# Optimization experiments

Hardware: AMD Instinct MI355X
Metric: run time of the kernel (lower is better)

## Reference

```python
import jax, jax.numpy as jnp
import numpy as np

MU = 1.0  # opts.loss_type[1]


def setup_inputs() -> dict:
    key = jax.random.key(0)
    k1, k2 = jax.random.split(key)
    B, D, N = 8, 3, 4096
    srcs = jax.random.normal(k1, (B, D, N), dtype=jnp.float32)
    tgts = jax.random.normal(k2, (B, D, N), dtype=jnp.float32)
    return {"srcs": srcs, "tgts": tgts}


def reference(srcs, tgts):
    # [B, D, N] -> [B, N, D]
    s = jnp.transpose(srcs, (0, 2, 1))
    t = jnp.transpose(tgts, (0, 2, 1))
    # squared euclidean pairwise distances: ||s_i - t_j||^2, [B, N, M]
    s_sq = jnp.sum(s * s, axis=-1)          # [B, N]
    t_sq = jnp.sum(t * t, axis=-1)          # [B, M]
    cross = jnp.einsum('bnd,bmd->bnm', s, t)  # [B, N, M]
    P = s_sq[:, :, None] + t_sq[:, None, :] - 2.0 * cross
    # bidirectional chamfer mins
    d_tgt = jnp.min(P, axis=1)  # min over src points, [B, M]
    d_src = jnp.min(P, axis=2)  # min over tgt points, [B, N]
    distances = jnp.stack([d_tgt, d_src], axis=-1)  # [B, N, 2]
    # Geman-McClure robust penalty
    losses = (MU * distances / (distances + MU)).sum(axis=2).mean(axis=1).mean()
    return losses
```

## Files before the change

### kernel.cpp

```cpp
#include <hip/hip_runtime.h>


#define NPTS 4096
#define NB   8

typedef __attribute__((ext_vector_type(8)))  short bf16x8;
typedef __attribute__((ext_vector_type(16))) float floatx16;

#define OFF_APACK_S 0u
#define OFF_APACK_T (1u << 20)
#define OFF_BPACK_S (2u << 20)
#define OFF_BPACK_T (3u << 20)
#define OFF_BSUM    (4u << 20)

union V16 { int4 i; bf16x8 h; };

__device__ __forceinline__ unsigned short f2bf(float f) {
    unsigned u = __float_as_uint(f);
    u += 0x7FFFu + ((u >> 16) & 1u);
    return (unsigned short)(u >> 16);
}
__device__ __forceinline__ float bf2f(unsigned short h) {
    return __uint_as_float(((unsigned)h) << 16);
}
__device__ __forceinline__ int pk(unsigned short lo, unsigned short hi) {
    return (int)((unsigned)lo | ((unsigned)hi << 16));
}

__device__ __forceinline__ void pack_point(const float* __restrict__ cloud,
                                           int b, int j, int gid,
                                           char* __restrict__ apack,
                                           char* __restrict__ bpack) {
    const unsigned short ONE = 0x3F80;
    const float* p = cloud + b * 3 * NPTS;
    const float x = p[j], y = p[NPTS + j], z = p[2 * NPTS + j];
    const unsigned short hx = f2bf(x), hy = f2bf(y), hz = f2bf(z);
    const unsigned short lx = f2bf(x - bf2f(hx));
    const unsigned short ly = f2bf(y - bf2f(hy));
    const unsigned short lz = f2bf(z - bf2f(hz));
    const unsigned short a0 = f2bf(-2.0f * bf2f(hx));
    const unsigned short a1 = f2bf(-2.0f * bf2f(hy));
    const unsigned short a2 = f2bf(-2.0f * bf2f(hz));
    const unsigned short m0 = f2bf(-2.0f * (x - bf2f(hx)));
    const unsigned short m1 = f2bf(-2.0f * (y - bf2f(hy)));
    const unsigned short m2 = f2bf(-2.0f * (z - bf2f(hz)));
    const float n2 = fmaf(z, z, fmaf(y, y, x * x));
    const unsigned short n2h = f2bf(n2);
    const unsigned short n2l = f2bf(n2 - bf2f(n2h));

    int4* Ap = (int4*)(apack + (size_t)gid * 32);
    Ap[0] = make_int4(pk(a0, a1), pk(a2, m0), pk(m1, m2), pk(a0, a1));
    Ap[1] = make_int4(pk(a2, n2h), pk(n2l, ONE), pk(ONE, 0), 0);

    int4* Bp = (int4*)(bpack + (size_t)gid * 32);
    Bp[0] = make_int4(pk(hx, hy), pk(hz, hx), pk(hy, hz), pk(lx, ly));
    Bp[1] = make_int4(pk(lz, ONE), pk(ONE, n2h), pk(n2l, 0), 0);
}

__global__ __launch_bounds__(256)
void transform_kernel(const float* __restrict__ srcs,
                      const float* __restrict__ tgts,
                      char* __restrict__ ws) {
    const int gid = blockIdx.x * 256 + threadIdx.x;
    const int b = gid >> 12, j = gid & 4095;
    pack_point(srcs, b, j, gid, ws + OFF_APACK_S, ws + OFF_BPACK_S);
    pack_point(tgts, b, j, gid, ws + OFF_APACK_T, ws + OFF_BPACK_T);
}

__global__ __launch_bounds__(512, 4)
void chamfer_kernel(char* __restrict__ ws) {
    const int blk    = blockIdx.x;
    const int dir    = blk >> 9;
    const int rem    = blk & 511;
    const int b      = rem >> 6;
    const int stripe = rem & 63;
    const int tid    = threadIdx.x;
    const int wave   = tid >> 6;
    const int lane   = tid & 63;
    const int l31    = lane & 31;
    const int half   = lane >> 5;

    const char* Ap = ws + (dir == 0 ? OFF_APACK_S : OFF_APACK_T);
    const char* Bp = ws + (dir == 0 ? OFF_BPACK_T : OFF_BPACK_S);

    V16 av0, av1;
    av0.i = *(const int4*)(Ap + (size_t)(b * NPTS + stripe * 64 + l31) * 32 + half * 16);
    av1.i = *(const int4*)(Ap + (size_t)(b * NPTS + stripe * 64 + 32 + l31) * 32 + half * 16);

    floatx16 rmin0, rmin1, zero;
#pragma unroll
    for (int r = 0; r < 16; r++) { rmin0[r] = 3.0e38f; rmin1[r] = 3.0e38f; zero[r] = 0.0f; }

    const int ct0 = wave * 16;
    const char* bbase = Bp + (size_t)(b * NPTS + ct0 * 32 + l31) * 32 + half * 16;

    V16 t0, t1, t2, t3;
    t0.i = *(const int4*)(bbase);
    t1.i = *(const int4*)(bbase + 1024);
    t2.i = *(const int4*)(bbase + 2048);
    t3.i = *(const int4*)(bbase + 3072);

#pragma unroll
    for (int i = 0; i < 16; i += 4) {
        V16 n0, n1, n2, n3;
        n0.i = *(const int4*)(bbase + (size_t)((i + 4) & 15) * 1024);
        n1.i = *(const int4*)(bbase + (size_t)((i + 5) & 15) * 1024);
        n2.i = *(const int4*)(bbase + (size_t)((i + 6) & 15) * 1024);
        n3.i = *(const int4*)(bbase + (size_t)((i + 7) & 15) * 1024);
#pragma unroll
        for (int u = 0; u < 4; u++) {
            const bf16x8 bf = (u == 0 ? t0.h : u == 1 ? t1.h : u == 2 ? t2.h : t3.h);
            const floatx16 d0 =
                __builtin_amdgcn_mfma_f32_32x32x16_bf16(av0.h, bf, zero, 0, 0, 0);
            const floatx16 d1 =
                __builtin_amdgcn_mfma_f32_32x32x16_bf16(av1.h, bf, zero, 0, 0, 0);
#pragma unroll
            for (int r = 0; r < 16; r++) {
                rmin0[r] = fminf(rmin0[r], d0[r]);
                rmin1[r] = fminf(rmin1[r], d1[r]);
            }
        }
        t0 = n0; t1 = n1; t2 = n2; t3 = n3;
    }

#pragma unroll
    for (int off = 1; off < 32; off <<= 1) {
#pragma unroll
        for (int r = 0; r < 16; r++) {
            rmin0[r] = fminf(rmin0[r], __shfl_xor(rmin0[r], off, 64));
            rmin1[r] = fminf(rmin1[r], __shfl_xor(rmin1[r], off, 64));
        }
    }
    __shared__ float sRow[8][64];
    if (l31 == 0) {
#pragma unroll
        for (int r = 0; r < 16; r++) {
            const int row = (r & 3) + 8 * (r >> 2) + 4 * half;
            sRow[wave][row]      = rmin0[r];
            sRow[wave][32 + row] = rmin1[r];
        }
    }
    __syncthreads();
    if (tid < 64) {
        float m = 3.0e38f;
#pragma unroll
        for (int w = 0; w < 8; w++) m = fminf(m, sRow[w][tid]);
        m = fmaxf(m, 0.0f);
        float g = m / (m + 1.0f);
#pragma unroll
        for (int off = 1; off < 64; off <<= 1)
            g += __shfl_xor(g, off, 64);
        if (tid == 0)
            ((float*)(ws + OFF_BSUM))[blk] = g;
    }
}

__global__ __launch_bounds__(256)
void finish_kernel(const char* __restrict__ ws, float* __restrict__ out) {
    const float* bsum = (const float*)(ws + OFF_BSUM);
    const int tid = threadIdx.x;
    float g = bsum[tid] + bsum[tid + 256] + bsum[tid + 512] + bsum[tid + 768];
#pragma unroll
    for (int off = 1; off < 64; off <<= 1)
        g += __shfl_xor(g, off, 64);
    __shared__ float sp[4];
    if ((tid & 63) == 0) sp[tid >> 6] = g;
    __syncthreads();
    if (tid == 0)
        out[0] = (sp[0] + sp[1] + sp[2] + sp[3]) * (1.0f / (NB * NPTS));
}

extern "C" void kernel_launch(void* const* d_in, const int* in_sizes, int n_in,
                              void* d_out, int out_size, void* d_ws, size_t ws_size,
                              hipStream_t stream) {
    const float* srcs = (const float*)d_in[0];
    const float* tgts = (const float*)d_in[1];
    float* out = (float*)d_out;
    char* ws = (char*)d_ws;

    transform_kernel<<<dim3(128), dim3(256), 0, stream>>>(srcs, tgts, ws);
    chamfer_kernel<<<dim3(1024), dim3(512), 0, stream>>>(ws);
    finish_kernel<<<dim3(1), dim3(256), 0, stream>>>(ws, out);
}
```

Measured before the change: 80.38 us.

## Halve row stripe per block and fuse final reduction via last-block atomics

Each chamfer block now covers 32 query points instead of 64, so the grid doubles to 2048 blocks and each wave issues one MFMA per column tile instead of two. The separate finish kernel is removed. Blocks atomically add partial sums into 64 cells, and the last block, detected with a ticket counter, reduces them and writes the output. This spreads work across more blocks and saves one launch, but the B tiles are now reloaded twice as often per query point and atomic contention is added.

```diff
diff --git a/kernel.cpp b/kernel.cpp
--- a/kernel.cpp
+++ b/kernel.cpp
@@ -11,7 +11,7 @@
 #define OFF_APACK_T (1u << 20)
 #define OFF_BPACK_S (2u << 20)
 #define OFF_BPACK_T (3u << 20)
-#define OFF_BSUM    (4u << 20)
+#define OFF_RED     (4u << 20)
 
 union V16 { int4 i; bf16x8 h; };
 
@@ -65,15 +65,17 @@
     const int b = gid >> 12, j = gid & 4095;
     pack_point(srcs, b, j, gid, ws + OFF_APACK_S, ws + OFF_BPACK_S);
     pack_point(tgts, b, j, gid, ws + OFF_APACK_T, ws + OFF_BPACK_T);
+    if (gid < 64)  ((float*)(ws + OFF_RED))[gid] = 0.0f;
+    if (gid == 64) *(unsigned*)(ws + OFF_RED + 256) = 0u;
 }
 
-__global__ __launch_bounds__(512, 4)
-void chamfer_kernel(char* __restrict__ ws) {
+__global__ __launch_bounds__(512)
+void chamfer_kernel(char* __restrict__ ws, float* __restrict__ out) {
     const int blk    = blockIdx.x;
-    const int dir    = blk >> 9;
-    const int rem    = blk & 511;
-    const int b      = rem >> 6;
-    const int stripe = rem & 63;
+    const int dir    = blk >> 10;
+    const int rem    = blk & 1023;
+    const int b      = rem >> 7;
+    const int stripe = rem & 127;
     const int tid    = threadIdx.x;
     const int wave   = tid >> 6;
     const int lane   = tid & 63;
@@ -82,14 +84,15 @@
 
     const char* Ap = ws + (dir == 0 ? OFF_APACK_S : OFF_APACK_T);
     const char* Bp = ws + (dir == 0 ? OFF_BPACK_T : OFF_BPACK_S);
+    float*    cells   = (float*)(ws + OFF_RED);
+    unsigned* gticket = (unsigned*)(ws + OFF_RED + 256);
 
-    V16 av0, av1;
-    av0.i = *(const int4*)(Ap + (size_t)(b * NPTS + stripe * 64 + l31) * 32 + half * 16);
-    av1.i = *(const int4*)(Ap + (size_t)(b * NPTS + stripe * 64 + 32 + l31) * 32 + half * 16);
+    V16 av;
+    av.i = *(const int4*)(Ap + (size_t)(b * NPTS + stripe * 32 + l31) * 32 + half * 16);
 
-    floatx16 rmin0, rmin1, zero;
+    floatx16 rmin, zero;
 #pragma unroll
-    for (int r = 0; r < 16; r++) { rmin0[r] = 3.0e38f; rmin1[r] = 3.0e38f; zero[r] = 0.0f; }
+    for (int r = 0; r < 16; r++) { rmin[r] = 3.0e38f; zero[r] = 0.0f; }
 
     const int ct0 = wave * 16;
     const char* bbase = Bp + (size_t)(b * NPTS + ct0 * 32 + l31) * 32 + half * 16;
@@ -110,15 +113,10 @@
 #pragma unroll
         for (int u = 0; u < 4; u++) {
             const bf16x8 bf = (u == 0 ? t0.h : u == 1 ? t1.h : u == 2 ? t2.h : t3.h);
-            const floatx16 d0 =
-                __builtin_amdgcn_mfma_f32_32x32x16_bf16(av0.h, bf, zero, 0, 0, 0);
-            const floatx16 d1 =
-                __builtin_amdgcn_mfma_f32_32x32x16_bf16(av1.h, bf, zero, 0, 0, 0);
+            const floatx16 d =
+                __builtin_amdgcn_mfma_f32_32x32x16_bf16(av.h, bf, zero, 0, 0, 0);
 #pragma unroll
-            for (int r = 0; r < 16; r++) {
-                rmin0[r] = fminf(rmin0[r], d0[r]);
-                rmin1[r] = fminf(rmin1[r], d1[r]);
-            }
+            for (int r = 0; r < 16; r++) rmin[r] = fminf(rmin[r], d[r]);
         }
         t0 = n0; t1 = n1; t2 = n2; t3 = n3;
     }
@@ -126,48 +124,46 @@
 #pragma unroll
     for (int off = 1; off < 32; off <<= 1) {
 #pragma unroll
-        for (int r = 0; r < 16; r++) {
-            rmin0[r] = fminf(rmin0[r], __shfl_xor(rmin0[r], off, 64));
-            rmin1[r] = fminf(rmin1[r], __shfl_xor(rmin1[r], off, 64));
-        }
+        for (int r = 0; r < 16; r++)
+            rmin[r] = fminf(rmin[r], __shfl_xor(rmin[r], off, 64));
     }
-    __shared__ float sRow[8][64];
+    __shared__ float sRow[8][32];
     if (l31 == 0) {
 #pragma unroll
-        for (int r = 0; r < 16; r++) {
-            const int row = (r & 3) + 8 * (r >> 2) + 4 * half;
-            sRow[wave][row]      = rmin0[r];
-            sRow[wave][32 + row] = rmin1[r];
-        }
+        for (int r = 0; r < 16; r++)
+            sRow[wave][(r & 3) + 8 * (r >> 2) + 4 * half] = rmin[r];
     }
     __syncthreads();
-    if (tid < 64) {
+
+    float g = 0.0f;
+    if (tid < 32) {
         float m = 3.0e38f;
 #pragma unroll
         for (int w = 0; w < 8; w++) m = fminf(m, sRow[w][tid]);
         m = fmaxf(m, 0.0f);
-        float g = m / (m + 1.0f);
+        g = m / (m + 1.0f);
 #pragma unroll
-        for (int off = 1; off < 64; off <<= 1)
+        for (int off = 1; off < 32; off <<= 1)
             g += __shfl_xor(g, off, 64);
-        if (tid == 0)
-            ((float*)(ws + OFF_BSUM))[blk] = g;
     }
-}
 
-__global__ __launch_bounds__(256)
-void finish_kernel(const char* __restrict__ ws, float* __restrict__ out) {
-    const float* bsum = (const float*)(ws + OFF_BSUM);
-    const int tid = threadIdx.x;
-    float g = bsum[tid] + bsum[tid + 256] + bsum[tid + 512] + bsum[tid + 768];
+    int last = 0;
+    if (tid == 0) {
+        atomicAdd(&cells[blk & 63], g);
+        __threadfence();
+        last = (atomicAdd(gticket, 1u) == 2047u) ? 1 : 0;
+    }
+    if (tid < 64) {
+        last = __shfl(last, 0, 64);
+        if (last) {
+            __threadfence();
+            float v = atomicAdd(&cells[tid], 0.0f);
 #pragma unroll
-    for (int off = 1; off < 64; off <<= 1)
-        g += __shfl_xor(g, off, 64);
-    __shared__ float sp[4];
-    if ((tid & 63) == 0) sp[tid >> 6] = g;
-    __syncthreads();
-    if (tid == 0)
-        out[0] = (sp[0] + sp[1] + sp[2] + sp[3]) * (1.0f / (NB * NPTS));
+            for (int off = 1; off < 64; off <<= 1)
+                v += __shfl_xor(v, off, 64);
+            if (tid == 0) out[0] = v * (1.0f / (NB * NPTS));
+        }
+    }
 }
 
 extern "C" void kernel_launch(void* const* d_in, const int* in_sizes, int n_in,
@@ -179,6 +175,5 @@
     char* ws = (char*)d_ws;
 
     transform_kernel<<<dim3(128), dim3(256), 0, stream>>>(srcs, tgts, ws);
-    chamfer_kernel<<<dim3(1024), dim3(512), 0, stream>>>(ws);
-    finish_kernel<<<dim3(1), dim3(256), 0, stream>>>(ws, out);
+    chamfer_kernel<<<dim3(2048), dim3(512), 0, stream>>>(ws, out);
 }
```

Result: slower. 123.6 us (+53.8%).
